# Kernel optimization log

Hardware: AMD Instinct MI355X
Metric: run time of the kernel (lower is better)

Reference implementation:

```python
import jax, jax.numpy as jnp
import numpy as np

# Problem sizes
N, D, B = 4096, 2048, 64  # nodes, feature dim, sequential samples
# LARFDSSOM hyperparameters (from __init__ defaults)
A_T = 0.3          # activation threshold
DSBETA = 1e-4      # moving-average rate
E_B = 0.5          # winner learning rate
E_N = 0.01 * E_B   # neighbor learning rate (e_n is multiplied by e_b in __init__)
EPS_DS = 0.01      # relevance smoothing


def setup_inputs() -> dict:
    key = jax.random.key(0)
    k0, k1, k2, k3, k4 = jax.random.split(key, 5)
    return {
        "x": jax.random.uniform(k0, (B, D), jnp.float32),
        "weights": jax.random.uniform(k1, (N, D), jnp.float32),
        "moving_avg": jax.random.uniform(k2, (N, D), jnp.float32),
        "relevances": jax.random.uniform(k3, (N, D), jnp.float32),
        "wins": jnp.zeros((N,), jnp.float32),
        "neighbors": jax.random.randint(k4, (N, N), 0, 2) > 0,
    }


def _som_steps(x, weights, moving_avg, relevances, wins, neighbors):
    """Sequential LARFDSSOM update_map over B samples (codebook at max size,
    so the add_node branch is structurally impossible and the per-sample step
    is either 'update winner + neighbors' or a no-op)."""
    node_ids = jnp.arange(weights.shape[0])

    def step(state, w):
        W, M, R, wn = state
        diff = w[None, :] - W                          # [N, D]
        # weighted_distance + activation
        dists = jnp.sum(R * diff * diff, axis=1)       # [N]
        rel_sum = jnp.sum(R, axis=1)                   # [N]
        act = rel_sum / (rel_sum + dists + 1e-7)
        winner = jnp.argmax(act)
        do_upd = act[winner] >= A_T                    # else no-op (codebook full)
        is_winner = node_ids == winner
        is_nb = neighbors[winner] & (~is_winner)
        # per-node learning rate: e_b for winner, e_n for neighbors, 0 otherwise
        lr = jnp.where(is_winner, E_B, jnp.where(is_nb, E_N, 0.0))[:, None]  # [N, 1]
        # update_node (vectorized over all nodes, masked below)
        dist_abs = jnp.abs(diff)
        M_new = lr * DSBETA * dist_abs + (1.0 - lr * DSBETA) * M
        mx = jnp.max(M_new, axis=1, keepdims=True)
        mn = jnp.min(M_new, axis=1, keepdims=True)
        av = jnp.mean(M_new, axis=1, keepdims=True)
        denom = EPS_DS * (mx - mn)
        # denom == 0 -> original produces NaN then sets relevance to 1.0
        arg = jnp.clip((M_new - av) / jnp.where(denom == 0.0, 1.0, denom), -80.0, 80.0)
        R_new = jnp.where(denom == 0.0, 1.0, 1.0 / (1.0 + jnp.exp(arg)))
        W_new = W + lr * diff
        m = (do_upd & (lr[:, 0] > 0.0))[:, None]       # rows actually touched
        W = jnp.where(m, W_new, W)
        M = jnp.where(m, M_new, M)
        R = jnp.where(m, R_new, R)
        wn = wn + jnp.where(is_winner & do_upd, 1.0, 0.0)
        return (W, M, R, wn), None

    (W, M, R, wn), _ = jax.lax.scan(step, (weights, moving_avg, relevances, wins), x)
    return W


def reference(x, weights, moving_avg, relevances, wins, neighbors):
    return _som_steps(x, weights, moving_avg, relevances, wins, neighbors)
```

## Files before the change

kernel.cpp:

```cpp
#include <hip/hip_runtime.h>
#include <cstddef>

#define NN 4096
#define DD 2048
#define BB 64
#define RPB 8
#define NBLK (NN / RPB)

constexpr float kAT     = 0.3f;
constexpr float kDSBETA = 1e-4f;
constexpr float kEB     = 0.5f;
constexpr float kEN     = 0.005f;
constexpr float kEPS    = 0.01f;

__device__ __forceinline__ float wave_sum_f(float v) {
#pragma unroll
    for (int o = 32; o; o >>= 1) v += __shfl_xor(v, o, 64);
    return v;
}
__device__ __forceinline__ double wave_sum_d(double v) {
#pragma unroll
    for (int o = 32; o; o >>= 1) v += __shfl_xor(v, o, 64);
    return v;
}
__device__ __forceinline__ float wave_max_f(float v) {
#pragma unroll
    for (int o = 32; o; o >>= 1) v = fmaxf(v, __shfl_xor(v, o, 64));
    return v;
}
__device__ __forceinline__ float wave_min_f(float v) {
#pragma unroll
    for (int o = 32; o; o >>= 1) v = fminf(v, __shfl_xor(v, o, 64));
    return v;
}
__device__ __forceinline__ unsigned long long wave_max_u64(unsigned long long v) {
#pragma unroll
    for (int o = 32; o; o >>= 1) {
        const unsigned long long u = __shfl_xor(v, o, 64);
        v = (u > v) ? u : v;
    }
    return v;
}

__global__ void detect_nb(const unsigned char* __restrict__ nb, unsigned* __restrict__ flag) {
    unsigned v = 0;
    const int i0 = threadIdx.x * 256;
    for (int i = 0; i < 256; i++) {
        const int idx = i0 + i;
        if ((idx & 3) != 0) v |= nb[idx];
    }
    if (v != 0) atomicOr(flag, 1u);
}

__global__ __launch_bounds__(256, 2) void som_persist(
    const float* __restrict__ x,
    const float* __restrict__ W0,
    const float* __restrict__ M0,
    const float* __restrict__ R0,
    const unsigned char* __restrict__ nbb,
    const unsigned* __restrict__ flag,
    float* __restrict__ Wout,
    unsigned long long* __restrict__ pkey)
{
    const int tid  = threadIdx.x;
    const int wid  = tid >> 6;
    const int lane = tid & 63;
    const int bid  = (int)blockIdx.x;
    const int n0   = bid * RPB;
    const int col  = tid * 8;

    __shared__ double sdd[2][RPB][4];
    __shared__ float  sf[3][RPB][4];
    __shared__ unsigned long long skk[RPB];
    __shared__ unsigned long long sKey;

    const bool nb_byte = (*flag != 0);
    const int* nbi = (const int*)nbb;

    float w[RPB][8], r[RPB][8], m[RPB][8], xcur[8];

#pragma unroll
    for (int row = 0; row < RPB; ++row) {
        const size_t base = (size_t)(n0 + row) * DD + col;
        *(float4*)(&w[row][0]) = *(const float4*)(W0 + base);
        *(float4*)(&w[row][4]) = *(const float4*)(W0 + base + 4);
        *(float4*)(&r[row][0]) = *(const float4*)(R0 + base);
        *(float4*)(&r[row][4]) = *(const float4*)(R0 + base + 4);
        *(float4*)(&m[row][0]) = *(const float4*)(M0 + base);
        *(float4*)(&m[row][4]) = *(const float4*)(M0 + base + 4);
    }
    *(float4*)(xcur)     = *(const float4*)(x + col);
    *(float4*)(xcur + 4) = *(const float4*)(x + col + 4);

    auto act_phase = [&](int slot) {
#pragma unroll
        for (int row = 0; row < RPB; ++row) {
            double pd = 0.0, ps = 0.0;
#pragma unroll
            for (int j = 0; j < 8; ++j) {
                const double d  = (double)xcur[j] - (double)w[row][j];
                const double rj = (double)r[row][j];
                pd += rj * d * d;
                ps += rj;
            }
            pd = wave_sum_d(pd); ps = wave_sum_d(ps);
            if (lane == 0) { sdd[0][row][wid] = pd; sdd[1][row][wid] = ps; }
        }
        __syncthreads();
        if (tid < RPB) {
            const int row = tid;
            const double td = sdd[0][row][0] + sdd[0][row][1] + sdd[0][row][2] + sdd[0][row][3];
            const double tr = sdd[1][row][0] + sdd[1][row][1] + sdd[1][row][2] + sdd[1][row][3];
            const double act = tr / (tr + td + 1e-7);
            const unsigned long long ab = (unsigned long long)__double_as_longlong(act);
            skk[row] = (ab & ~0xFFFULL) | (unsigned long long)(4095 - (n0 + row));
        }
        __syncthreads();
        if (tid == 0) {
            unsigned long long k = skk[0];
#pragma unroll
            for (int i = 1; i < RPB; ++i) k = (skk[i] > k) ? skk[i] : k;
            __hip_atomic_store(&pkey[(size_t)slot * NBLK + bid], k,
                               __ATOMIC_RELAXED, __HIP_MEMORY_SCOPE_AGENT);
        }
    };

    act_phase(0);

    float xn[8];
    for (int t = 0; t < BB; ++t) {
        const bool has_next = (t < BB - 1);
        if (has_next) {
            const size_t xb = (size_t)(t + 1) * DD + col;
            *(float4*)(xn)     = *(const float4*)(x + xb);
            *(float4*)(xn + 4) = *(const float4*)(x + xb + 4);
        }

        if (wid == 0) {
            unsigned long long* pk = pkey + (size_t)t * NBLK;
            unsigned long long kk[8];
            int it = 0;
            while (true) {
                bool miss = false;
#pragma unroll
                for (int i = 0; i < 8; ++i) {
                    kk[i] = __hip_atomic_load(&pk[lane + 64 * i],
                                              __ATOMIC_RELAXED, __HIP_MEMORY_SCOPE_AGENT);
                    miss |= (kk[i] == 0ull);
                }
                if (!__any(miss)) break;
                if (++it > 2000000) break;
                __builtin_amdgcn_s_sleep(1);
            }
            unsigned long long kmax = 0;
#pragma unroll
            for (int i = 0; i < 8; ++i) kmax = (kk[i] > kmax) ? kk[i] : kmax;
            kmax = wave_max_u64(kmax);
            if (lane == 0) sKey = kmax;
        }
        __syncthreads();
        const unsigned long long k = sKey;
        const double act_w = __longlong_as_double((long long)(k & ~0xFFFULL));
        const int winner   = 4095 - (int)(k & 0xFFFULL);

        if (act_w >= (double)kAT) {
            int nbr[RPB];
            {
                const size_t off = (size_t)winner * NN + n0;
                if (nb_byte) {
                    const unsigned long long nb8 = *(const unsigned long long*)(nbb + off);
#pragma unroll
                    for (int i = 0; i < RPB; ++i)
                        nbr[i] = (int)((nb8 >> (8 * i)) & 0xFFull);
                } else {
                    const int4 a = *(const int4*)(nbi + off);
                    const int4 b = *(const int4*)(nbi + off + 4);
                    nbr[0] = a.x; nbr[1] = a.y; nbr[2] = a.z; nbr[3] = a.w;
                    nbr[4] = b.x; nbr[5] = b.y; nbr[6] = b.z; nbr[7] = b.w;
                }
            }
            float lrs[RPB];
            bool any = false;
#pragma unroll
            for (int row = 0; row < RPB; ++row) {
                const int n = n0 + row;
                float lr = 0.0f;
                if (n == winner)      lr = kEB;
                else if (nbr[row])    lr = kEN;
                lrs[row] = lr;
                if (lr != 0.0f) {
                    any = true;
                    const float c1 = lr * kDSBETA;
                    const float c2 = 1.0f - c1;
                    float psum = 0.0f, pmx = -INFINITY, pmn = INFINITY;
#pragma unroll
                    for (int j = 0; j < 8; ++j) {
                        const float d  = xcur[j] - w[row][j];
                        const float mv = c1 * fabsf(d) + c2 * m[row][j];
                        w[row][j] += lr * d;
                        m[row][j] = mv;
                        psum += mv;
                        pmx = fmaxf(pmx, mv);
                        pmn = fminf(pmn, mv);
                    }
                    psum = wave_sum_f(psum); pmx = wave_max_f(pmx); pmn = wave_min_f(pmn);
                    if (lane == 0) { sf[0][row][wid] = psum; sf[1][row][wid] = pmx; sf[2][row][wid] = pmn; }
                }
            }
            if (any) {
                __syncthreads();
#pragma unroll
                for (int row = 0; row < RPB; ++row) {
                    if (lrs[row] != 0.0f) {
                        const float ts  = sf[0][row][0] + sf[0][row][1] + sf[0][row][2] + sf[0][row][3];
                        const float tmx = fmaxf(fmaxf(sf[1][row][0], sf[1][row][1]),
                                                fmaxf(sf[1][row][2], sf[1][row][3]));
                        const float tmn = fminf(fminf(sf[2][row][0], sf[2][row][1]),
                                                fminf(sf[2][row][2], sf[2][row][3]));
                        const float av    = ts * (1.0f / (float)DD);
                        const float denom = kEPS * (tmx - tmn);
                        if (denom == 0.0f) {
#pragma unroll
                            for (int j = 0; j < 8; ++j) r[row][j] = 1.0f;
                        } else {
#pragma unroll
                            for (int j = 0; j < 8; ++j) {
                                float a = (m[row][j] - av) / denom;
                                a = fminf(fmaxf(a, -80.0f), 80.0f);
                                r[row][j] = 1.0f / (1.0f + expf(a));
                            }
                        }
                    }
                }
            }
        }

        if (has_next) {
#pragma unroll
            for (int j = 0; j < 8; ++j) xcur[j] = xn[j];
            act_phase(t + 1);
        }
    }

#pragma unroll
    for (int row = 0; row < RPB; ++row) {
        const size_t base = (size_t)(n0 + row) * DD + col;
        *(float4*)(Wout + base)     = *(float4*)(&w[row][0]);
        *(float4*)(Wout + base + 4) = *(float4*)(&w[row][4]);
    }
}

__global__ __launch_bounds__(256) void som_step(
    const float* __restrict__ x_upd, const float* __restrict__ x_act,
    float* __restrict__ W, float* __restrict__ M, float* __restrict__ R,
    const void* __restrict__ nb, const unsigned* __restrict__ flag,
    const unsigned long long* __restrict__ part_upd,
    unsigned long long* __restrict__ part_act)
{
    const int n   = blockIdx.x;
    const int tid = threadIdx.x;
    __shared__ float  sred[3][4];
    __shared__ double sredd[2][4];

    float lr = 0.0f;
    if (part_upd != nullptr) {
        unsigned long long k = part_upd[(size_t)(tid & 63) * 8];
        k = wave_max_u64(k);
        const double act_w = __longlong_as_double((long long)(k & ~0xFFFULL));
        const int winner   = 4095 - (int)(k & 0xFFFULL);
        if (act_w >= (double)kAT) {
            if (n == winner) lr = kEB;
            else {
                const size_t off = (size_t)winner * NN + n;
                const bool isnb = (*flag != 0)
                    ? (((const unsigned char*)nb)[off] != 0)
                    : (((const int*)nb)[off] != 0);
                if (isnb) lr = kEN;
            }
        }
    }
    const bool next = (x_act != nullptr);
    if (lr == 0.0f && !next) return;

    const size_t rowoff = (size_t)n * DD + (size_t)tid * 8;
    const size_t xoff   = (size_t)tid * 8;
    float w[8], r[8];
    *(float4*)(w)     = *(const float4*)(W + rowoff);
    *(float4*)(w + 4) = *(const float4*)(W + rowoff + 4);

    if (lr != 0.0f) {
        float m[8], xu[8], mnew[8];
        *(float4*)(m)      = *(const float4*)(M + rowoff);
        *(float4*)(m + 4)  = *(const float4*)(M + rowoff + 4);
        *(float4*)(xu)     = *(const float4*)(x_upd + xoff);
        *(float4*)(xu + 4) = *(const float4*)(x_upd + xoff + 4);
        const float c1 = lr * kDSBETA, c2 = 1.0f - c1;
        float psum = 0.0f, pmx = -INFINITY, pmn = INFINITY;
#pragma unroll
        for (int j = 0; j < 8; j++) {
            const float d = xu[j] - w[j];
            w[j] += lr * d;
            const float mv = c1 * fabsf(d) + c2 * m[j];
            mnew[j] = mv; psum += mv;
            pmx = fmaxf(pmx, mv); pmn = fminf(pmn, mv);
        }
        psum = wave_sum_f(psum); pmx = wave_max_f(pmx); pmn = wave_min_f(pmn);
        const int wid = tid >> 6, lane = tid & 63;
        if (lane == 0) { sred[0][wid] = psum; sred[1][wid] = pmx; sred[2][wid] = pmn; }
        __syncthreads();
        const float ts  = sred[0][0] + sred[0][1] + sred[0][2] + sred[0][3];
        const float tmx = fmaxf(fmaxf(sred[1][0], sred[1][1]), fmaxf(sred[1][2], sred[1][3]));
        const float tmn = fminf(fminf(sred[2][0], sred[2][1]), fminf(sred[2][2], sred[2][3]));
        __syncthreads();
        const float av = ts * (1.0f / (float)DD);
        const float denom = kEPS * (tmx - tmn);
        if (denom == 0.0f) {
#pragma unroll
            for (int j = 0; j < 8; j++) r[j] = 1.0f;
        } else {
#pragma unroll
            for (int j = 0; j < 8; j++) {
                float a = (mnew[j] - av) / denom;
                a = fminf(fmaxf(a, -80.0f), 80.0f);
                r[j] = 1.0f / (1.0f + expf(a));
            }
        }
        *(float4*)(W + rowoff)     = *(float4*)(w);
        *(float4*)(W + rowoff + 4) = *(float4*)(w + 4);
        *(float4*)(M + rowoff)     = *(float4*)(mnew);
        *(float4*)(M + rowoff + 4) = *(float4*)(mnew + 4);
        *(float4*)(R + rowoff)     = *(float4*)(r);
        *(float4*)(R + rowoff + 4) = *(float4*)(r + 4);
    } else {
        *(float4*)(r)     = *(const float4*)(R + rowoff);
        *(float4*)(r + 4) = *(const float4*)(R + rowoff + 4);
    }

    if (next) {
        float xn[8];
        *(float4*)(xn)     = *(const float4*)(x_act + xoff);
        *(float4*)(xn + 4) = *(const float4*)(x_act + xoff + 4);
        double pd = 0.0, ps = 0.0;
#pragma unroll
        for (int j = 0; j < 8; j++) {
            const double d  = (double)xn[j] - (double)w[j];
            const double rj = (double)r[j];
            pd += rj * d * d; ps += rj;
        }
        pd = wave_sum_d(pd); ps = wave_sum_d(ps);
        const int wid = tid >> 6, lane = tid & 63;
        if (lane == 0) { sredd[0][wid] = pd; sredd[1][wid] = ps; }
        __syncthreads();
        if (tid == 0) {
            const double td = sredd[0][0] + sredd[0][1] + sredd[0][2] + sredd[0][3];
            const double tr = sredd[1][0] + sredd[1][1] + sredd[1][2] + sredd[1][3];
            const double act = tr / (tr + td + 1e-7);
            const unsigned long long ab = (unsigned long long)__double_as_longlong(act);
            const unsigned long long kk = (ab & ~0xFFFULL) | (unsigned long long)(4095 - n);
            atomicMax(&part_act[(size_t)(n & 63) * 8], kk);
        }
    }
}

extern "C" void kernel_launch(void* const* d_in, const int* in_sizes, int n_in,
                              void* d_out, int out_size, void* d_ws, size_t ws_size,
                              hipStream_t stream) {
    const float*         x   = (const float*)d_in[0];
    const float*         W0  = (const float*)d_in[1];
    float*               M   = (float*)d_in[2];
    float*               R   = (float*)d_in[3];
    const unsigned char* nbb = (const unsigned char*)d_in[5];
    float*               W   = (float*)d_out;

    unsigned long long* part = (unsigned long long*)d_ws;
    const size_t part_bytes  = (size_t)66 * 64 * 8 * sizeof(unsigned long long);
    const size_t cnt_bytes = (size_t)BB * 8 * 16 * sizeof(unsigned);
    unsigned* flagp = (unsigned*)((char*)d_ws + part_bytes + cnt_bytes);

    hipMemsetAsync(d_ws, 0, part_bytes + cnt_bytes + 64, stream);
    detect_nb<<<1, 256, 0, stream>>>(nbb, flagp);

    int occ = 0;
    hipError_t qerr = hipOccupancyMaxActiveBlocksPerMultiprocessor(
        &occ, (const void*)som_persist, 256, 0);
    if (qerr == hipSuccess && occ >= 2) {
        som_persist<<<NBLK, 256, 0, stream>>>(x, W0, M, R, nbb, flagp, W, part);
        return;
    }

    hipMemcpyAsync(W, W0, sizeof(float) * (size_t)NN * DD, hipMemcpyDeviceToDevice, stream);
    som_step<<<NN, 256, 0, stream>>>(nullptr, x, W, M, R, nbb, flagp, nullptr, part);
    for (int t = 0; t < BB; t++) {
        const float* xu = x + (size_t)t * DD;
        const float* xa = (t < BB - 1) ? (x + (size_t)(t + 1) * DD) : nullptr;
        const unsigned long long* pu = part + (size_t)t * 64 * 8;
        unsigned long long*       pa = (t < BB - 1) ? (part + (size_t)(t + 1) * 64 * 8) : nullptr;
        som_step<<<NN, 256, 0, stream>>>(xu, xa, W, M, R, nbb, flagp, pu, pa);
    }
}
```

Baseline: 1.681 ms.

## Use two-level grid winner reduction and skip relevance-sum recompute for untouched rows

Replaces the flat barrier, where every block polled all 512 per-block keys, with a two-level scheme. One leader block per group of 8 reduces its group's keys into a group-key array, and all blocks then poll only the 64 group keys. The per-block act reduction now uses a wave shuffle instead of an extra __syncthreads. The relevance row-sum is recomputed only for rows updated in the previous step, with cached values kept in shared memory. This cuts global polling traffic and per-step work, at the cost of an extra dependency hop through the leader blocks.

```diff
diff --git a/kernel.cpp b/kernel.cpp
--- a/kernel.cpp
+++ b/kernel.cpp
@@ -6,6 +6,7 @@
 #define BB 64
 #define RPB 8
 #define NBLK (NN / RPB)
+#define NGRP (NBLK / 8)
 
 constexpr float kAT     = 0.3f;
 constexpr float kDSBETA = 1e-4f;
@@ -60,7 +61,8 @@
     const unsigned char* __restrict__ nbb,
     const unsigned* __restrict__ flag,
     float* __restrict__ Wout,
-    unsigned long long* __restrict__ pkey)
+    unsigned long long* __restrict__ pkey,
+    unsigned long long* __restrict__ gkey)
 {
     const int tid  = threadIdx.x;
     const int wid  = tid >> 6;
@@ -68,10 +70,12 @@
     const int bid  = (int)blockIdx.x;
     const int n0   = bid * RPB;
     const int col  = tid * 8;
-
-    __shared__ double sdd[2][RPB][4];
+    const int grp  = bid >> 3;
+    const bool leader = ((bid & 7) == 0);
+
+    __shared__ double sdd[RPB][4];
+    __shared__ double spp[RPB][4];
     __shared__ float  sf[3][RPB][4];
-    __shared__ unsigned long long skk[RPB];
     __shared__ unsigned long long sKey;
 
     const bool nb_byte = (*flag != 0);
@@ -92,40 +96,47 @@
     *(float4*)(xcur)     = *(const float4*)(x + col);
     *(float4*)(xcur + 4) = *(const float4*)(x + col + 4);
 
-    auto act_phase = [&](int slot) {
+    auto act_phase = [&](int slot, unsigned touched) {
 #pragma unroll
         for (int row = 0; row < RPB; ++row) {
-            double pd = 0.0, ps = 0.0;
+            const bool doPs = (touched >> row) & 1u;
+            double pd = 0.0;
 #pragma unroll
             for (int j = 0; j < 8; ++j) {
                 const double d  = (double)xcur[j] - (double)w[row][j];
                 const double rj = (double)r[row][j];
                 pd += rj * d * d;
-                ps += rj;
-            }
-            pd = wave_sum_d(pd); ps = wave_sum_d(ps);
-            if (lane == 0) { sdd[0][row][wid] = pd; sdd[1][row][wid] = ps; }
+            }
+            pd = wave_sum_d(pd);
+            if (lane == 0) sdd[row][wid] = pd;
+            if (doPs) {
+                double ps = 0.0;
+#pragma unroll
+                for (int j = 0; j < 8; ++j) ps += (double)r[row][j];
+                ps = wave_sum_d(ps);
+                if (lane == 0) spp[row][wid] = ps;
+            }
         }
         __syncthreads();
-        if (tid < RPB) {
-            const int row = tid;
-            const double td = sdd[0][row][0] + sdd[0][row][1] + sdd[0][row][2] + sdd[0][row][3];
-            const double tr = sdd[1][row][0] + sdd[1][row][1] + sdd[1][row][2] + sdd[1][row][3];
+        if (wid == 0 && lane < RPB) {
+            const int row = lane;
+            const double td = sdd[row][0] + sdd[row][1] + sdd[row][2] + sdd[row][3];
+            const double tr = spp[row][0] + spp[row][1] + spp[row][2] + spp[row][3];
             const double act = tr / (tr + td + 1e-7);
             const unsigned long long ab = (unsigned long long)__double_as_longlong(act);
-            skk[row] = (ab & ~0xFFFULL) | (unsigned long long)(4095 - (n0 + row));
-        }
-        __syncthreads();
-        if (tid == 0) {
-            unsigned long long k = skk[0];
-#pragma unroll
-            for (int i = 1; i < RPB; ++i) k = (skk[i] > k) ? skk[i] : k;
-            __hip_atomic_store(&pkey[(size_t)slot * NBLK + bid], k,
-                               __ATOMIC_RELAXED, __HIP_MEMORY_SCOPE_AGENT);
+            unsigned long long k = (ab & ~0xFFFULL) | (unsigned long long)(4095 - (n0 + row));
+#pragma unroll
+            for (int o = 1; o < RPB; o <<= 1) {
+                const unsigned long long u = __shfl_xor(k, o, 64);
+                k = (u > k) ? u : k;
+            }
+            if (lane == 0)
+                __hip_atomic_store(&pkey[(size_t)slot * NBLK + bid], k,
+                                   __ATOMIC_RELAXED, __HIP_MEMORY_SCOPE_AGENT);
         }
     };
 
-    act_phase(0);
+    act_phase(0, 0xFFu);
 
     float xn[8];
     for (int t = 0; t < BB; ++t) {
@@ -137,32 +148,49 @@
         }
 
         if (wid == 0) {
-            unsigned long long* pk = pkey + (size_t)t * NBLK;
-            unsigned long long kk[8];
-            int it = 0;
-            while (true) {
-                bool miss = false;
-#pragma unroll
-                for (int i = 0; i < 8; ++i) {
-                    kk[i] = __hip_atomic_load(&pk[lane + 64 * i],
+            if (leader) {
+                if (lane < 8) {
+                    unsigned long long* pk = pkey + (size_t)t * NBLK + (grp << 3);
+                    unsigned long long v;
+                    int it = 0;
+                    while (true) {
+                        v = __hip_atomic_load(&pk[lane],
                                               __ATOMIC_RELAXED, __HIP_MEMORY_SCOPE_AGENT);
-                    miss |= (kk[i] == 0ull);
+                        if (!__any(v == 0ull)) break;
+                        if (++it > 2000000) break;
+                        __builtin_amdgcn_s_sleep(2);
+                    }
+#pragma unroll
+                    for (int o = 1; o < 8; o <<= 1) {
+                        const unsigned long long u = __shfl_xor(v, o, 64);
+                        v = (u > v) ? u : v;
+                    }
+                    if (lane == 0)
+                        __hip_atomic_store(&gkey[(size_t)t * NGRP + grp], v,
+                                           __ATOMIC_RELAXED, __HIP_MEMORY_SCOPE_AGENT);
                 }
-                if (!__any(miss)) break;
-                if (++it > 2000000) break;
-                __builtin_amdgcn_s_sleep(1);
-            }
-            unsigned long long kmax = 0;
-#pragma unroll
-            for (int i = 0; i < 8; ++i) kmax = (kk[i] > kmax) ? kk[i] : kmax;
-            kmax = wave_max_u64(kmax);
-            if (lane == 0) sKey = kmax;
+            }
+            unsigned long long kv;
+            {
+                unsigned long long* gk = gkey + (size_t)t * NGRP;
+                int it = 0;
+                while (true) {
+                    kv = __hip_atomic_load(&gk[lane],
+                                           __ATOMIC_RELAXED, __HIP_MEMORY_SCOPE_AGENT);
+                    if (!__any(kv == 0ull)) break;
+                    if (++it > 2000000) break;
+                    __builtin_amdgcn_s_sleep(4);
+                }
+            }
+            kv = wave_max_u64(kv);
+            if (lane == 0) sKey = kv;
         }
         __syncthreads();
         const unsigned long long k = sKey;
         const double act_w = __longlong_as_double((long long)(k & ~0xFFFULL));
         const int winner   = 4095 - (int)(k & 0xFFFULL);
 
+        unsigned touched = 0u;
         if (act_w >= (double)kAT) {
             int nbr[RPB];
             {
@@ -180,7 +208,6 @@
                 }
             }
             float lrs[RPB];
-            bool any = false;
 #pragma unroll
             for (int row = 0; row < RPB; ++row) {
                 const int n = n0 + row;
@@ -189,7 +216,7 @@
                 else if (nbr[row])    lr = kEN;
                 lrs[row] = lr;
                 if (lr != 0.0f) {
-                    any = true;
+                    touched |= (1u << row);
                     const float c1 = lr * kDSBETA;
                     const float c2 = 1.0f - c1;
                     float psum = 0.0f, pmx = -INFINITY, pmn = INFINITY;
@@ -207,7 +234,7 @@
                     if (lane == 0) { sf[0][row][wid] = psum; sf[1][row][wid] = pmx; sf[2][row][wid] = pmn; }
                 }
             }
-            if (any) {
+            if (touched) {
                 __syncthreads();
 #pragma unroll
                 for (int row = 0; row < RPB; ++row) {
@@ -238,7 +265,7 @@
         if (has_next) {
 #pragma unroll
             for (int j = 0; j < 8; ++j) xcur[j] = xn[j];
-            act_phase(t + 1);
+            act_phase(t + 1, touched);
         }
     }
 
@@ -374,6 +401,7 @@
 
     unsigned long long* part = (unsigned long long*)d_ws;
     const size_t part_bytes  = (size_t)66 * 64 * 8 * sizeof(unsigned long long);
+    unsigned long long* gkey = (unsigned long long*)((char*)d_ws + part_bytes);
     const size_t cnt_bytes = (size_t)BB * 8 * 16 * sizeof(unsigned);
     unsigned* flagp = (unsigned*)((char*)d_ws + part_bytes + cnt_bytes);
 
@@ -384,7 +412,7 @@
     hipError_t qerr = hipOccupancyMaxActiveBlocksPerMultiprocessor(
         &occ, (const void*)som_persist, 256, 0);
     if (qerr == hipSuccess && occ >= 2) {
-        som_persist<<<NBLK, 256, 0, stream>>>(x, W0, M, R, nbb, flagp, W, part);
+        som_persist<<<NBLK, 256, 0, stream>>>(x, W0, M, R, nbb, flagp, W, part, gkey);
         return;
     }
 
```

Measured after the change: 1.695 ms. Within noise of the previous version (+0.8%).
